# Kernel tuning notes

Measured on AMD Instinct MI355X. Metric: run time of the kernel, lower is better.

Reference implementation:

```python
import jax, jax.numpy as jnp
import numpy as np

B, S, D, H, DFF, NB = 32, 512, 256, 8, 1024, 2
L = NB + 2 * NB  # 2 blocks_1 + 4 blocks_2 = 6 layers, params stacked on axis 0
DK = D // H
NEG = jnp.float32(-1e32)


def _ln(x, s, b):
    mu = jnp.mean(x, -1, keepdims=True)
    var = jnp.mean((x - mu) ** 2, -1, keepdims=True)
    return (x - mu) * jax.lax.rsqrt(var + 1e-5) * s + b


def _attn(q, k, v, gamma, mask, zero_pad):
    # q,k,v: [B,H,S,DK]; mask: [1,1,S,S] bool; gamma: [H,1,1]
    scores = jnp.einsum('bhid,bhjd->bhij', q, k) / jnp.float32(np.sqrt(DK))
    # distance-decay effect (computed with no grad in the original)
    sc = jax.nn.softmax(jnp.where(mask, scores, NEG), axis=-1) * mask
    cum = jnp.cumsum(sc, axis=-1)
    tot = jnp.sum(sc, axis=-1, keepdims=True)
    idx = jnp.arange(S, dtype=jnp.float32)
    pos = jnp.abs(idx[None, :] - idx[:, None])[None, None]  # |i-j|
    dist = jax.lax.stop_gradient(jnp.sqrt(jnp.maximum((tot - cum) * pos, 0.0)))
    g = -jax.nn.softplus(gamma)[None]  # [1,H,1,1]
    eff = jnp.clip(jnp.exp(dist * g), 1e-5, 1e5)
    scores = jnp.where(mask, scores * eff, NEG)
    a = jax.nn.softmax(scores, axis=-1)
    if zero_pad:
        a = a.at[:, :, 0, :].set(0.0)
    return jnp.einsum('bhij,bhjd->bhid', a, v)


def _layer(i, mask_flag, q, k, v, apply_pos,
           Wk, bk, Wv, bv, Wo, bo, gammas, ln1_s, ln1_b, W1, b1, W2, b2, ln2_s, ln2_b):
    diag = 0 if mask_flag == 1 else -1  # mask=1: incl. diag; mask=0: strictly past
    mask = jnp.tril(jnp.ones((S, S), bool), diag)[None, None]
    to_h = lambda x, W, bb: (x @ W + bb).reshape(B, S, H, DK).transpose(0, 2, 1, 3)
    qh = to_h(q, Wk[i], bk[i])  # kq_same=True -> q uses k_linear
    kh = to_h(k, Wk[i], bk[i])
    vh = to_h(v, Wv[i], bv[i])
    o = _attn(qh, kh, vh, gammas[i], mask, zero_pad=(mask_flag == 0))
    o = o.transpose(0, 2, 1, 3).reshape(B, S, D) @ Wo[i] + bo[i]
    q = _ln(q + o, ln1_s[i], ln1_b[i])
    if apply_pos:
        f = jax.nn.relu(q @ W1[i] + b1[i]) @ W2[i] + b2[i]
        q = _ln(q + f, ln2_s[i], ln2_b[i])
    return q


def _forward(q_embed_data, qa_embed_data, *p):
    y, x = qa_embed_data, q_embed_data
    for i in range(NB):
        y = _layer(i, 1, y, y, y, True, *p)
    flag = True
    for j in range(2 * NB):
        i = NB + j
        if flag:
            x = _layer(i, 1, x, x, x, False, *p)
        else:
            x = _layer(i, 0, x, x, y, True, *p)
        flag = not flag
    return x


def setup_inputs() -> dict:
    key = jax.random.key(0)
    ks = jax.random.split(key, 9)
    sd = jnp.float32(1.0 / np.sqrt(D))
    sdf = jnp.float32(1.0 / np.sqrt(DFF))
    xb = float(np.sqrt(3.0))  # xavier bound for gammas (fan_in=fan_out=1)
    return {
        'q_embed_data': jax.random.normal(ks[0], (B, S, D), jnp.float32),
        'qa_embed_data': jax.random.normal(ks[1], (B, S, D), jnp.float32),
        'Wk': jax.random.normal(ks[2], (L, D, D), jnp.float32) * sd,
        'bk': jnp.zeros((L, D), jnp.float32),
        'Wv': jax.random.normal(ks[3], (L, D, D), jnp.float32) * sd,
        'bv': jnp.zeros((L, D), jnp.float32),
        'Wo': jax.random.normal(ks[4], (L, D, D), jnp.float32) * sd,
        'bo': jnp.zeros((L, D), jnp.float32),
        'gammas': jax.random.uniform(ks[5], (L, H, 1, 1), jnp.float32, -xb, xb),
        'ln1_s': jnp.ones((L, D), jnp.float32),
        'ln1_b': jnp.zeros((L, D), jnp.float32),
        'W1': jax.random.normal(ks[6], (L, D, DFF), jnp.float32) * sd,
        'b1': jnp.zeros((L, DFF), jnp.float32),
        'W2': jax.random.normal(ks[7], (L, DFF, D), jnp.float32) * sdf,
        'b2': jnp.zeros((L, D), jnp.float32),
        'ln2_s': jnp.ones((L, D), jnp.float32),
        'ln2_b': jnp.zeros((L, D), jnp.float32),
    }


def reference(q_embed_data, qa_embed_data, Wk, bk, Wv, bv, Wo, bo, gammas,
              ln1_s, ln1_b, W1, b1, W2, b2, ln2_s, ln2_b):
    return _forward(q_embed_data, qa_embed_data, Wk, bk, Wv, bv, Wo, bo, gammas,
                    ln1_s, ln1_b, W1, b1, W2, b2, ln2_s, ln2_b)
```

## Files before the change

### kernel.cpp

```cpp
#include <hip/hip_runtime.h>
#include <cstdint>
#include <cstddef>


#define AS1 __attribute__((address_space(1)))
#define AS3 __attribute__((address_space(3)))

typedef __bf16 bf16;
typedef __bf16 bf16x8 __attribute__((ext_vector_type(8)));
typedef __bf16 bf16x4 __attribute__((ext_vector_type(4)));
typedef __bf16 bf16x2 __attribute__((ext_vector_type(2)));
typedef float  f32x4  __attribute__((ext_vector_type(4)));
typedef float  f32x16 __attribute__((ext_vector_type(16)));
typedef unsigned int u32;

static constexpr int Mc = 32 * 512;

__global__ void cvt_copy2_kernel(const float* __restrict__ s0, float* __restrict__ da32,
                                 bf16* __restrict__ da16, const float* __restrict__ s1,
                                 float* __restrict__ db32, bf16* __restrict__ db16, int n4) {
  const float* s = blockIdx.y ? s1 : s0;
  float* d32 = blockIdx.y ? db32 : da32;
  bf16* d16 = blockIdx.y ? db16 : da16;
  int i = blockIdx.x * blockDim.x + threadIdx.x;
  if (i < n4) {
    float4 v = ((const float4*)s)[i];
    ((float4*)d32)[i] = v;
    bf16x4 hx = {(bf16)v.x, (bf16)v.y, (bf16)v.z, (bf16)v.w};
    ((bf16x4*)d16)[i] = hx;
  }
}

__global__ __launch_bounds__(256) void transpose_cvt_all(
    const float* __restrict__ Wk, const float* __restrict__ Wv, const float* __restrict__ Wo,
    const float* __restrict__ W1, const float* __restrict__ W2,
    bf16* __restrict__ Wkt, bf16* __restrict__ Wvt, bf16* __restrict__ Wot,
    bf16* __restrict__ W1t, bf16* __restrict__ W2t) {
  int z = blockIdx.z;
  int layer = z % 6, w = z / 6;
  const float* src; bf16* dst; int K, N;
  switch (w) {
    case 0: src = Wk; dst = Wkt; K = 256; N = 256; break;
    case 1: src = Wv; dst = Wvt; K = 256; N = 256; break;
    case 2: src = Wo; dst = Wot; K = 256; N = 256; break;
    case 3: src = W1; dst = W1t; K = 256; N = 1024; break;
    default: src = W2; dst = W2t; K = 1024; N = 256; break;
  }
  int k0 = blockIdx.x * 64, n0 = blockIdx.y * 64;
  if (k0 >= K || n0 >= N) return;
  src += (size_t)layer * K * N;
  dst += (size_t)layer * K * N;
  __shared__ bf16 t[64][68];
  int tid = threadIdx.x;
  int rr = tid >> 4;
  int c4 = (tid & 15) * 4;
#pragma unroll
  for (int p = 0; p < 4; ++p) {
    int k = rr + p * 16;
    float4 v = *(const float4*)(src + (size_t)(k0 + k) * N + n0 + c4);
    t[c4 + 0][k] = (bf16)v.x;
    t[c4 + 1][k] = (bf16)v.y;
    t[c4 + 2][k] = (bf16)v.z;
    t[c4 + 3][k] = (bf16)v.w;
  }
  __syncthreads();
#pragma unroll
  for (int p = 0; p < 4; ++p) {
    int nl = rr + p * 16;
    bf16x4 o4 = *(const bf16x4*)&t[nl][c4];
    *(bf16x4*)(dst + (size_t)(n0 + nl) * K + k0 + c4) = o4;
  }
}

template <int RELU, typename OUT_T>
__device__ __forceinline__ void gemm_body(
    const bf16* __restrict__ A, const bf16* __restrict__ Bt,
    const float* __restrict__ bias, OUT_T* __restrict__ C,
    int K, int N, int m0, int n0, bf16* As, bf16* Bs) {
  const int tid = threadIdx.x;
  const int lane = tid & 63;
  const int wid = tid >> 6;
  const int wm = (wid >> 1) * 64;
  const int wn = (wid & 1) * 64;
  f32x4 acc[4][4] = {};

  const int o1 = wid * 1024 + lane * 16;
  const int o2 = o1 + 4096;
  const int r1 = o1 >> 6, c1 = o1 & 63;
  const int r2 = o2 >> 6, c2 = o2 & 63;
  const char* Ab = (const char*)A;
  const char* Bb = (const char*)Bt;
  const size_t stride = (size_t)K * 2;

  auto stage_panel = [&](int panel, int kk) {
    const char* a1 = Ab + (size_t)(m0 + r1) * stride + (size_t)kk * 2 + c1;
    const char* a2 = Ab + (size_t)(m0 + r2) * stride + (size_t)kk * 2 + c2;
    const char* b1 = Bb + (size_t)(n0 + r1) * stride + (size_t)kk * 2 + c1;
    const char* b2 = Bb + (size_t)(n0 + r2) * stride + (size_t)kk * 2 + c2;
    char* ad = (char*)As + panel * 8192 + wid * 1024;
    char* bd = (char*)Bs + panel * 8192 + wid * 1024;
    __builtin_amdgcn_global_load_lds((const AS1 u32*)a1, (AS3 u32*)ad, 16, 0, 0);
    __builtin_amdgcn_global_load_lds((const AS1 u32*)a2, (AS3 u32*)(ad + 4096), 16, 0, 0);
    __builtin_amdgcn_global_load_lds((const AS1 u32*)b1, (AS3 u32*)bd, 16, 0, 0);
    __builtin_amdgcn_global_load_lds((const AS1 u32*)b2, (AS3 u32*)(bd + 4096), 16, 0, 0);
  };

  stage_panel(0, 0);
  stage_panel(1, 32);
  asm volatile("s_waitcnt vmcnt(0)" ::: "memory");
  __syncthreads();

  int cur = 0;
  for (int k0 = 0; k0 < K; k0 += 64) {
    if (k0 + 64 < K) {
      stage_panel((cur ^ 1) * 2, k0 + 64);
      stage_panel((cur ^ 1) * 2 + 1, k0 + 96);
    }
    const int rr = lane & 15;
    const int g8 = (lane >> 4) * 8;
#pragma unroll
    for (int s = 0; s < 2; ++s) {
      const int base = (cur * 2 + s) * 4096;
      bf16x8 af[4], bfr[4];
#pragma unroll
      for (int i = 0; i < 4; ++i) {
        af[i]  = *(const bf16x8*)&As[base + (wm + i * 16 + rr) * 32 + g8];
        bfr[i] = *(const bf16x8*)&Bs[base + (wn + i * 16 + rr) * 32 + g8];
      }
#pragma unroll
      for (int mi = 0; mi < 4; ++mi)
#pragma unroll
        for (int ni = 0; ni < 4; ++ni)
          acc[mi][ni] = __builtin_amdgcn_mfma_f32_16x16x32_bf16(af[mi], bfr[ni], acc[mi][ni], 0, 0, 0);
    }
    asm volatile("s_waitcnt vmcnt(0)" ::: "memory");
    __syncthreads();
    cur ^= 1;
  }

  const int rr = lane & 15;
  const int g4 = (lane >> 4) * 4;
  float bv[4];
#pragma unroll
  for (int ni = 0; ni < 4; ++ni) bv[ni] = bias[n0 + wn + ni * 16 + rr];
#pragma unroll
  for (int mi = 0; mi < 4; ++mi)
#pragma unroll
    for (int ni = 0; ni < 4; ++ni)
#pragma unroll
      for (int r = 0; r < 4; ++r) {
        float v = acc[mi][ni][r] + bv[ni];
        if (RELU) v = fmaxf(v, 0.f);
        int row = m0 + wm + mi * 16 + g4 + r;
        int col = n0 + wn + ni * 16 + rr;
        C[(size_t)row * N + col] = (OUT_T)v;
      }
}

__global__ __launch_bounds__(256) void gemm_kv_kernel(
    const bf16* __restrict__ A0, const bf16* __restrict__ Bt0,
    const float* __restrict__ b0, bf16* __restrict__ C0,
    const bf16* __restrict__ A1, const bf16* __restrict__ Bt1,
    const float* __restrict__ b1, bf16* __restrict__ C1, int K, int N) {
  __shared__ bf16 As[4 * 4096];
  __shared__ bf16 Bs[4 * 4096];
  int sel = blockIdx.y >> 1;
  gemm_body<0, bf16>(sel ? A1 : A0, sel ? Bt1 : Bt0, sel ? b1 : b0, sel ? C1 : C0,
                     K, N, blockIdx.x * 128, (blockIdx.y & 1) * 128, As, Bs);
}

template <int KSZ>
__global__ __launch_bounds__(512, 4) void gemm_ln_kernel(
    const bf16* __restrict__ A, const bf16* __restrict__ Bt,
    const float* __restrict__ bias, const float* __restrict__ resid,
    const float* __restrict__ lns, const float* __restrict__ lnb,
    float* __restrict__ out32, bf16* __restrict__ out16) {
  __shared__ bf16 As[2 * 32 * 32];
  __shared__ bf16 Bs[2 * 256 * 32];
  __shared__ float wsum[8][16][2];
  __shared__ float stats[32][2];
  const int tid = threadIdx.x, lane = tid & 63, wid = tid >> 6;
  const int m0 = blockIdx.x * 32;
  const int wr = wid >> 2, wc = wid & 3;
  f32x4 acc[4] = {};
  const char* Ab = (const char*)A;
  const char* Bb = (const char*)Bt;
  const size_t stride = (size_t)KSZ * 2;

  auto stage = [&](int buf, int kk) {
    if (wid < 2) {
      int off = wid * 1024 + lane * 16;
      const char* a1 = Ab + (size_t)(m0 + (off >> 6)) * stride + (size_t)kk * 2 + (off & 63);
      __builtin_amdgcn_global_load_lds((const AS1 u32*)a1,
                                       (AS3 u32*)((char*)As + buf * 2048 + wid * 1024), 16, 0, 0);
    }
    int off1 = wid * 2048 + lane * 16;
    int off2 = off1 + 1024;
    const char* b1 = Bb + (size_t)(off1 >> 6) * stride + (size_t)kk * 2 + (off1 & 63);
    const char* b2 = Bb + (size_t)(off2 >> 6) * stride + (size_t)kk * 2 + (off2 & 63);
    char* bd = (char*)Bs + buf * 16384 + wid * 2048;
    __builtin_amdgcn_global_load_lds((const AS1 u32*)b1, (AS3 u32*)bd, 16, 0, 0);
    __builtin_amdgcn_global_load_lds((const AS1 u32*)b2, (AS3 u32*)(bd + 1024), 16, 0, 0);
  };

  stage(0, 0);
  asm volatile("s_waitcnt vmcnt(0)" ::: "memory");
  __syncthreads();

  int cur = 0;
  for (int k0 = 0; k0 < KSZ; k0 += 32) {
    if (k0 + 32 < KSZ) stage(cur ^ 1, k0 + 32);
    const int rr = lane & 15, g8 = (lane >> 4) * 8;
    bf16x8 af = *(const bf16x8*)&As[cur * 1024 + (wr * 16 + rr) * 32 + g8];
    bf16x8 bfr[4];
#pragma unroll
    for (int ni = 0; ni < 4; ++ni)
      bfr[ni] = *(const bf16x8*)&Bs[cur * 8192 + (wc * 64 + ni * 16 + rr) * 32 + g8];
#pragma unroll
    for (int ni = 0; ni < 4; ++ni)
      acc[ni] = __builtin_amdgcn_mfma_f32_16x16x32_bf16(af, bfr[ni], acc[ni], 0, 0, 0);
    asm volatile("s_waitcnt vmcnt(0)" ::: "memory");
    __syncthreads();
    cur ^= 1;
  }

  const int rr = lane & 15, g4 = (lane >> 4) * 4;
  float bv[4], scv[4], biv[4];
  int col[4];
#pragma unroll
  for (int ni = 0; ni < 4; ++ni) {
    col[ni] = wc * 64 + ni * 16 + rr;
    bv[ni] = bias[col[ni]];
    scv[ni] = lns[col[ni]];
    biv[ni] = lnb[col[ni]];
  }
  float v[4][4];
#pragma unroll
  for (int r = 0; r < 4; ++r) {
    int grow = m0 + wr * 16 + g4 + r;
#pragma unroll
    for (int ni = 0; ni < 4; ++ni)
      v[ni][r] = acc[ni][r] + bv[ni] + resid[(size_t)grow * 256 + col[ni]];
  }
#pragma unroll
  for (int r = 0; r < 4; ++r) {
    float s1 = (v[0][r] + v[1][r]) + (v[2][r] + v[3][r]);
    float s2 = (v[0][r] * v[0][r] + v[1][r] * v[1][r]) + (v[2][r] * v[2][r] + v[3][r] * v[3][r]);
#pragma unroll
    for (int off = 8; off; off >>= 1) {
      s1 += __shfl_xor(s1, off);
      s2 += __shfl_xor(s2, off);
    }
    if (rr == 0) {
      int lrow = wr * 16 + g4 + r;
      wsum[wid][lrow & 15][0] = s1;
      wsum[wid][lrow & 15][1] = s2;
    }
  }
  __syncthreads();
  if (tid < 32) {
    int row = tid;
    int band = row >> 4;
    float s1 = 0.f, s2 = 0.f;
#pragma unroll
    for (int k = 0; k < 4; ++k) {
      s1 += wsum[band * 4 + k][row & 15][0];
      s2 += wsum[band * 4 + k][row & 15][1];
    }
    float mu = s1 * (1.f / 256.f);
    float var = s2 * (1.f / 256.f) - mu * mu;
    stats[row][0] = mu;
    stats[row][1] = rsqrtf(var + 1e-5f);
  }
  __syncthreads();
#pragma unroll
  for (int r = 0; r < 4; ++r) {
    int lrow = wr * 16 + g4 + r;
    int grow = m0 + lrow;
    float mu = stats[lrow][0], rs = stats[lrow][1];
#pragma unroll
    for (int ni = 0; ni < 4; ++ni) {
      float y = (v[ni][r] - mu) * rs * scv[ni] + biv[ni];
      out32[(size_t)grow * 256 + col[ni]] = y;
      out16[(size_t)grow * 256 + col[ni]] = (bf16)y;
    }
  }
}

__global__ __launch_bounds__(1024, 4) void gemm_ln_ffn_kernel(
    const bf16* __restrict__ A, const bf16* __restrict__ Bt,
    const float* __restrict__ bias, const float* __restrict__ resid,
    const float* __restrict__ lns, const float* __restrict__ lnb,
    const bf16* __restrict__ W1t, const float* __restrict__ b1,
    const bf16* __restrict__ W2t, const float* __restrict__ b2,
    const float* __restrict__ ln2s, const float* __restrict__ ln2b,
    float* __restrict__ out32, bf16* __restrict__ out16) {
  __shared__ bf16 As[2 * 4096];
  __shared__ bf16 Bs[2 * 16384];
  __shared__ bf16 vL[64 * 264];
  __shared__ bf16 hch[64 * 264];
  __shared__ float wsum[16][16][2];
  __shared__ float stats[64][2];
  const int tid = threadIdx.x, lane = tid & 63, wid = tid >> 6;
  const int m0 = blockIdx.x * 64;
  const int wr = wid >> 2, wc = wid & 3;
  const int rr = lane & 15, g4 = (lane >> 4) * 4, g8 = (lane >> 4) * 8;
  const int g = lane >> 4;
  const char* Ab = (const char*)A;
  const char* Bb = (const char*)Bt;
  const size_t strideA = 512;
  const size_t strideW1 = 512;
  const size_t strideW2 = 2048;

  int col[4];
#pragma unroll
  for (int ni = 0; ni < 4; ++ni) col[ni] = wc * 64 + ni * 16 + rr;

  auto stageA = [&](int kk, int buf) {
    if (wid < 8) {
      int cp = wid * 64 + lane;
      int cl = cp ^ ((cp >> 3) & 7);
      int row = cl >> 3, gq = cl & 7;
      const char* a1 = Ab + (size_t)(m0 + row) * strideA + (size_t)kk * 2 + gq * 16;
      __builtin_amdgcn_global_load_lds((const AS1 u32*)a1,
                                       (AS3 u32*)((char*)As + buf * 8192 + cp * 16), 16, 0, 0);
    }
  };
  auto stageB = [&](const char* Wb, size_t strideB, int rbase, int kk, int buf) {
#pragma unroll
    for (int j = 0; j < 2; ++j) {
      int cp = wid * 128 + j * 64 + lane;
      int cl = cp ^ ((cp >> 3) & 7);
      int row = cl >> 3, gq = cl & 7;
      const char* b1p = Wb + (size_t)(rbase + row) * strideB + (size_t)kk * 2 + gq * 16;
      __builtin_amdgcn_global_load_lds((const AS1 u32*)b1p,
                                       (AS3 u32*)((char*)Bs + buf * 32768 + cp * 16), 16, 0, 0);
    }
  };
  auto breadB = [&](int buf, int nrow, int s) -> bf16x8 {
    int cb = nrow * 8 + s * 4 + g;
    int cs = cb ^ (nrow & 7);
    return *(const bf16x8*)&Bs[buf * 16384 + cs * 8];
  };
  auto areadA = [&](int buf, int nrow, int s) -> bf16x8 {
    int cb = nrow * 8 + s * 4 + g;
    int cs = cb ^ (nrow & 7);
    return *(const bf16x8*)&As[buf * 4096 + cs * 8];
  };

  f32x4 acc[4] = {};
  stageA(0, 0);
  stageB(Bb, strideA, 0, 0, 0);
  {
    int cur = 0;
    for (int k0 = 0; k0 < 256; k0 += 64) {
      const bool pf = (k0 + 64 < 256);
      if (pf) {
        stageA(k0 + 64, cur ^ 1);
        stageB(Bb, strideA, 0, k0 + 64, cur ^ 1);
        if (wid < 8) asm volatile("s_waitcnt vmcnt(3)" ::: "memory");
        else         asm volatile("s_waitcnt vmcnt(2)" ::: "memory");
      } else {
        asm volatile("s_waitcnt vmcnt(0)" ::: "memory");
      }
      __builtin_amdgcn_s_barrier();
      __builtin_amdgcn_sched_barrier(0);
#pragma unroll
      for (int s = 0; s < 2; ++s) {
        bf16x8 af = areadA(cur, wr * 16 + rr, s);
        bf16x8 bfr[4];
#pragma unroll
        for (int ni = 0; ni < 4; ++ni)
          bfr[ni] = breadB(cur, wc * 64 + ni * 16 + rr, s);
#pragma unroll
        for (int ni = 0; ni < 4; ++ni)
          acc[ni] = __builtin_amdgcn_mfma_f32_16x16x32_bf16(af, bfr[ni], acc[ni], 0, 0, 0);
      }
      __builtin_amdgcn_sched_barrier(0);
      __builtin_amdgcn_s_barrier();
      cur ^= 1;
    }
  }

  float y[4][4];
  {
    float bv[4], scv[4], biv[4];
#pragma unroll
    for (int ni = 0; ni < 4; ++ni) {
      bv[ni] = bias[col[ni]];
      scv[ni] = lns[col[ni]];
      biv[ni] = lnb[col[ni]];
    }
    float v[4][4];
#pragma unroll
    for (int r = 0; r < 4; ++r) {
      int grow = m0 + wr * 16 + g4 + r;
#pragma unroll
      for (int ni = 0; ni < 4; ++ni)
        v[ni][r] = acc[ni][r] + bv[ni] + resid[(size_t)grow * 256 + col[ni]];
    }
#pragma unroll
    for (int r = 0; r < 4; ++r) {
      float s1 = (v[0][r] + v[1][r]) + (v[2][r] + v[3][r]);
      float s2 = (v[0][r] * v[0][r] + v[1][r] * v[1][r]) + (v[2][r] * v[2][r] + v[3][r] * v[3][r]);
#pragma unroll
      for (int off = 8; off; off >>= 1) {
        s1 += __shfl_xor(s1, off);
        s2 += __shfl_xor(s2, off);
      }
      if (rr == 0) {
        wsum[wid][g4 + r][0] = s1;
        wsum[wid][g4 + r][1] = s2;
      }
    }
    __syncthreads();
    if (tid < 64) {
      int row = tid;
      int band = row >> 4;
      float s1 = 0.f, s2 = 0.f;
#pragma unroll
      for (int k = 0; k < 4; ++k) {
        s1 += wsum[band * 4 + k][row & 15][0];
        s2 += wsum[band * 4 + k][row & 15][1];
      }
      float mu = s1 * (1.f / 256.f);
      float var = s2 * (1.f / 256.f) - mu * mu;
      stats[row][0] = mu;
      stats[row][1] = rsqrtf(var + 1e-5f);
    }
    __syncthreads();
#pragma unroll
    for (int r = 0; r < 4; ++r) {
      int lrow = wr * 16 + g4 + r;
      float mu = stats[lrow][0], rs = stats[lrow][1];
#pragma unroll
      for (int ni = 0; ni < 4; ++ni) {
        float yy = (v[ni][r] - mu) * rs * scv[ni] + biv[ni];
        y[ni][r] = yy;
        vL[lrow * 264 + col[ni]] = (bf16)yy;
      }
    }
  }
  __syncthreads();

  const char* W1b = (const char*)W1t;
  const char* W2b = (const char*)W2t;
  f32x4 acc2[4] = {};

  for (int nb = 0; nb < 4; ++nb) {
    f32x4 acc1[4] = {};
    stageB(W1b, strideW1, nb * 256, 0, 0);
    {
      int cur = 0;
      for (int k0 = 0; k0 < 256; k0 += 64) {
        const bool pf = (k0 + 64 < 256);
        if (pf) {
          stageB(W1b, strideW1, nb * 256, k0 + 64, cur ^ 1);
          asm volatile("s_waitcnt vmcnt(2)" ::: "memory");
        } else {
          asm volatile("s_waitcnt vmcnt(0)" ::: "memory");
        }
        __builtin_amdgcn_s_barrier();
        __builtin_amdgcn_sched_barrier(0);
#pragma unroll
        for (int s = 0; s < 2; ++s) {
          bf16x8 af = *(const bf16x8*)&vL[(wr * 16 + rr) * 264 + k0 + s * 32 + g8];
          bf16x8 bfr[4];
#pragma unroll
          for (int ni = 0; ni < 4; ++ni)
            bfr[ni] = breadB(cur, wc * 64 + ni * 16 + rr, s);
#pragma unroll
          for (int ni = 0; ni < 4; ++ni)
            acc1[ni] = __builtin_amdgcn_mfma_f32_16x16x32_bf16(af, bfr[ni], acc1[ni], 0, 0, 0);
        }
        __builtin_amdgcn_sched_barrier(0);
        __builtin_amdgcn_s_barrier();
        cur ^= 1;
      }
    }
#pragma unroll
    for (int ni = 0; ni < 4; ++ni) {
      float bb = b1[nb * 256 + col[ni]];
#pragma unroll
      for (int r = 0; r < 4; ++r) {
        int lrow = wr * 16 + g4 + r;
        hch[lrow * 264 + col[ni]] = (bf16)fmaxf(acc1[ni][r] + bb, 0.f);
      }
    }
    __syncthreads();

    stageB(W2b, strideW2, 0, nb * 256, 0);
    {
      int cur = 0;
      for (int k0 = 0; k0 < 256; k0 += 64) {
        const bool pf = (k0 + 64 < 256);
        if (pf) {
          stageB(W2b, strideW2, 0, nb * 256 + k0 + 64, cur ^ 1);
          asm volatile("s_waitcnt vmcnt(2)" ::: "memory");
        } else {
          asm volatile("s_waitcnt vmcnt(0)" ::: "memory");
        }
        __builtin_amdgcn_s_barrier();
        __builtin_amdgcn_sched_barrier(0);
#pragma unroll
        for (int s = 0; s < 2; ++s) {
          bf16x8 af = *(const bf16x8*)&hch[(wr * 16 + rr) * 264 + k0 + s * 32 + g8];
          bf16x8 bfr[4];
#pragma unroll
          for (int ni = 0; ni < 4; ++ni)
            bfr[ni] = breadB(cur, wc * 64 + ni * 16 + rr, s);
#pragma unroll
          for (int ni = 0; ni < 4; ++ni)
            acc2[ni] = __builtin_amdgcn_mfma_f32_16x16x32_bf16(af, bfr[ni], acc2[ni], 0, 0, 0);
        }
        __builtin_amdgcn_sched_barrier(0);
        __builtin_amdgcn_s_barrier();
        cur ^= 1;
      }
    }
    __syncthreads();
  }

  {
    float bv[4], scv[4], biv[4];
#pragma unroll
    for (int ni = 0; ni < 4; ++ni) {
      bv[ni] = b2[col[ni]];
      scv[ni] = ln2s[col[ni]];
      biv[ni] = ln2b[col[ni]];
    }
    float v[4][4];
#pragma unroll
    for (int r = 0; r < 4; ++r)
#pragma unroll
      for (int ni = 0; ni < 4; ++ni)
        v[ni][r] = y[ni][r] + acc2[ni][r] + bv[ni];
#pragma unroll
    for (int r = 0; r < 4; ++r) {
      float s1 = (v[0][r] + v[1][r]) + (v[2][r] + v[3][r]);
      float s2 = (v[0][r] * v[0][r] + v[1][r] * v[1][r]) + (v[2][r] * v[2][r] + v[3][r] * v[3][r]);
#pragma unroll
      for (int off = 8; off; off >>= 1) {
        s1 += __shfl_xor(s1, off);
        s2 += __shfl_xor(s2, off);
      }
      if (rr == 0) {
        wsum[wid][g4 + r][0] = s1;
        wsum[wid][g4 + r][1] = s2;
      }
    }
    __syncthreads();
    if (tid < 64) {
      int row = tid;
      int band = row >> 4;
      float s1 = 0.f, s2 = 0.f;
#pragma unroll
      for (int k = 0; k < 4; ++k) {
        s1 += wsum[band * 4 + k][row & 15][0];
        s2 += wsum[band * 4 + k][row & 15][1];
      }
      float mu = s1 * (1.f / 256.f);
      float var = s2 * (1.f / 256.f) - mu * mu;
      stats[row][0] = mu;
      stats[row][1] = rsqrtf(var + 1e-5f);
    }
    __syncthreads();
#pragma unroll
    for (int r = 0; r < 4; ++r) {
      int lrow = wr * 16 + g4 + r;
      int grow = m0 + lrow;
      float mu = stats[lrow][0], rs = stats[lrow][1];
#pragma unroll
      for (int ni = 0; ni < 4; ++ni) {
        float yy = (v[ni][r] - mu) * rs * scv[ni] + biv[ni];
        out32[(size_t)grow * 256 + col[ni]] = yy;
        out16[(size_t)grow * 256 + col[ni]] = (bf16)yy;
      }
    }
  }
}

static constexpr int LDK = 34;
static constexpr int LDV = 534;
static constexpr float LOG2E = 1.4426950408889634f;
static constexpr float KSC = 0.17677669529663687f * LOG2E;

__device__ __forceinline__ int jloc(int r, int hi) { return (r & 3) + 8 * (r >> 2) + 4 * hi; }

__device__ __forceinline__ u32 pkbf(float x, float y) {
  bf16x2 t = {(bf16)x, (bf16)y};
  return __builtin_bit_cast(u32, t);
}

__device__ __forceinline__ void plswap(u32& a, u32& b) {
  asm volatile("v_permlane32_swap_b32 %0, %1" : "+v"(a), "+v"(b));
}

__device__ __forceinline__ f32x16 qk_tile(const bf16* Klds, int jbase, int lq,
                                          const bf16x8& qf0, const bf16x8& qf1, int hi) {
  const bf16x8 ka0 = *(const bf16x8*)&Klds[(jbase + lq) * LDK + hi * 8];
  const bf16x8 ka1 = *(const bf16x8*)&Klds[(jbase + lq) * LDK + 16 + hi * 8];
  f32x16 c = {};
  c = __builtin_amdgcn_mfma_f32_32x32x16_bf16(ka0, qf0, c, 0, 0, 0);
  c = __builtin_amdgcn_mfma_f32_32x32x16_bf16(ka1, qf1, c, 0, 0, 0);
  return c;
}

template <bool MASKED>
__device__ __forceinline__ void tileA(const f32x16& c, int jbase, int hi, int qlim, float& tot) {
  float t[4] = {0.f, 0.f, 0.f, 0.f};
#pragma unroll
  for (int q2 = 0; q2 < 4; ++q2)
#pragma unroll
    for (int p = 0; p < 4; ++p) {
      const int r = q2 * 4 + p;
      float e = __builtin_amdgcn_exp2f(c[r] * KSC);
      if (MASKED) {
        int j = jbase + 8 * q2 + 4 * hi + p;
        if (j > qlim) e = 0.f;
      }
      t[q2] += e;
    }
  tot += (t[0] + t[1]) + (t[2] + t[3]);
}

template <bool MASKED>
__device__ __forceinline__ void tileB(const f32x16& c, int jbase, int lq, int hi,
                                      int qlim, float itot, float gneg2, float posf,
                                      const bf16* Vt, float& run, float& sum2, f32x16& pvacc) {
  float su2[16], lcs[16], G[4];
#pragma unroll
  for (int q2 = 0; q2 < 4; ++q2) {
    float a = 0.f;
#pragma unroll
    for (int p = 0; p < 4; ++p) {
      const int r = q2 * 4 + p;
      su2[r] = c[r] * KSC;
      float e = __builtin_amdgcn_exp2f(su2[r]);
      if (MASKED) {
        int j = jbase + 8 * q2 + 4 * hi + p;
        if (j > qlim) e = 0.f;
      }
      a += e;
      lcs[r] = a;
    }
    G[q2] = a;
  }
  float Po[4];
#pragma unroll
  for (int q2 = 0; q2 < 4; ++q2) Po[q2] = __shfl_xor(G[q2], 32);
  float base[4];
  {
    float pre = run;
#pragma unroll
    for (int q2 = 0; q2 < 4; ++q2) {
      base[q2] = pre + (hi ? Po[q2] : 0.f);
      pre += G[q2] + Po[q2];
    }
    run = pre;
  }
#pragma unroll
  for (int cc = 0; cc < 2; ++cc) {
    float pv[8];
#pragma unroll
    for (int q2s = 0; q2s < 2; ++q2s) {
      const int q2 = cc * 2 + q2s;
#pragma unroll
      for (int p = 0; p < 4; ++p) {
        const int r = q2 * 4 + p;
        float cum = base[q2] + lcs[r];
        float pos = posf - (float)(8 * q2 + p);
        float d2 = fmaxf(__builtin_fmaf(-cum, itot, 1.f) * pos, 0.f);
        float dist = __builtin_amdgcn_sqrtf(d2);
        float eff = fmaxf(__builtin_amdgcn_exp2f(dist * gneg2), 1e-5f);
        float t = __builtin_amdgcn_exp2f(su2[r] * eff);
        if (MASKED) {
          int j = jbase + 8 * q2 + 4 * hi + p;
          if (j > qlim) t = 0.f;
        }
        pv[q2s * 4 + p] = t;
      }
    }
    sum2 += ((pv[0] + pv[1]) + (pv[2] + pv[3])) + ((pv[4] + pv[5]) + (pv[6] + pv[7]));
    u32 a0 = pkbf(pv[0], pv[1]);
    u32 a1 = pkbf(pv[2], pv[3]);
    u32 b0 = pkbf(pv[4], pv[5]);
    u32 b1 = pkbf(pv[6], pv[7]);
    plswap(a0, b0);
    plswap(a1, b1);
    uint4 fq; fq.x = a0; fq.y = a1; fq.z = b0; fq.w = b1;
    bf16x8 pa = __builtin_bit_cast(bf16x8, fq);
    bf16x8 vb = *(const bf16x8*)&Vt[(size_t)lq * LDV + jbase + cc * 16 + hi * 8];
    pvacc = __builtin_amdgcn_mfma_f32_32x32x16_bf16(pa, vb, pvacc, 0, 0, 0);
  }
}

__global__ __launch_bounds__(1024, 4) void attn_kernel(
    const bf16* __restrict__ kh, const bf16* __restrict__ vh,
    const float* __restrict__ gam, bf16* __restrict__ o, int incl_diag) {
  __shared__ bf16 Klds[512 * LDK];
  __shared__ bf16 Vt[32 * LDV];
  __shared__ float exA[8][32];
  __shared__ float exB[8][32];
  __shared__ float s2A[8][32];
  __shared__ float pvp[8][32][32];

  const int tid = threadIdx.x;
  const int lane = tid & 63;
  const int wid = tid >> 6;
  const int bh = blockIdx.x;
  const int b = bh >> 3, h = bh & 7;
  const bf16* kbase = kh + ((size_t)b * 4096 + h) * 32;
  const bf16* vbase = vh + ((size_t)b * 4096 + h) * 32;
  bf16* obase = o + ((size_t)b * 4096 + h) * 32;

#pragma unroll
  for (int it = 0; it < 2; ++it) {
    int t = it * 1024 + tid;
    int j = t >> 2, cc = t & 3;
    bf16x8 kv8 = *(const bf16x8*)(kbase + (size_t)j * 256 + cc * 8);
    *(bf16x8*)&Klds[j * LDK + cc * 8] = kv8;
  }
  {
    int u = tid & 255;
    int cg = tid >> 8;
    const bf16* vb = vbase + (size_t)(2 * u) * 256 + cg * 8;
    bf16x8 r0 = *(const bf16x8*)(vb);
    bf16x8 r1 = *(const bf16x8*)(vb + 256);
#pragma unroll
    for (int e = 0; e < 8; ++e) {
      bf16x2 w2 = {r0[e], r1[e]};
      *(bf16x2*)&Vt[(size_t)(cg * 8 + e) * LDV + 2 * u] = w2;
    }
  }
  __syncthreads();

  float gm = gam[h];
  float gneg = -(fmaxf(gm, 0.f) + log1pf(__expf(-fabsf(gm))));
  const float gneg2 = gneg * LOG2E;
  const int lq = lane & 31;
  const int hi = lane >> 5;

  const int p = wid & 7;
  const bool front = wid < 8;
  const int f = 7 - p;
  const int qbHi = 15 - p;
  const int ntHi = 16 - p;
  const int q0Hi = qbHi * 32;
  const int qrHi = q0Hi + lq;
  const int qlimHi = incl_diag ? qrHi : qrHi - 1;
  const int q0Lo = p * 32;
  const int qrLo = q0Lo + lq;
  const int qlimLo = incl_diag ? qrLo : qrLo - 1;

  const bf16x8 qfH0 = *(const bf16x8*)&Klds[(q0Hi + lq) * LDK + hi * 8];
  const bf16x8 qfH1 = *(const bf16x8*)&Klds[(q0Hi + lq) * LDK + 16 + hi * 8];

  float totLo = 0.f, S = 0.f;
  if (front) {
    const bf16x8 qfL0 = *(const bf16x8*)&Klds[(q0Lo + lq) * LDK + hi * 8];
    const bf16x8 qfL1 = *(const bf16x8*)&Klds[(q0Lo + lq) * LDK + 16 + hi * 8];
    for (int jt = 0; jt < p; ++jt) {
      f32x16 c = qk_tile(Klds, jt * 32, lq, qfL0, qfL1, hi);
      tileA<false>(c, jt * 32, hi, qlimLo, totLo);
    }
    {
      f32x16 c = qk_tile(Klds, q0Lo, lq, qfL0, qfL1, hi);
      tileA<true>(c, q0Lo, hi, qlimLo, totLo);
    }
    totLo += __shfl_xor(totLo, 32);
    for (int jt = 0; jt < f; ++jt) {
      f32x16 c = qk_tile(Klds, jt * 32, lq, qfH0, qfH1, hi);
      tileA<false>(c, jt * 32, hi, qlimHi, S);
    }
    S += __shfl_xor(S, 32);
    if (lane < 32) exA[p][lq] = S;
  } else {
    for (int jt = f; jt < ntHi - 1; ++jt) {
      f32x16 c = qk_tile(Klds, jt * 32, lq, qfH0, qfH1, hi);
      tileA<false>(c, jt * 32, hi, qlimHi, S);
    }
    {
      f32x16 c = qk_tile(Klds, q0Hi, lq, qfH0, qfH1, hi);
      tileA<true>(c, q0Hi, hi, qlimHi, S);
    }
    S += __shfl_xor(S, 32);
    if (lane < 32) exB[p][lq] = S;
  }
  __syncthreads();
  const float SA = exA[p][lq];
  const float SB = exB[p][lq];
  const float totHi = SA + SB;
  const float itotHi = totHi > 0.f ? 1.f / totHi : 0.f;

  f32x16 pvHi = {};
  float sum2Hi = 0.f;
  if (front) {
    const bf16x8 qfL0 = *(const bf16x8*)&Klds[(q0Lo + lq) * LDK + hi * 8];
    const bf16x8 qfL1 = *(const bf16x8*)&Klds[(q0Lo + lq) * LDK + 16 + hi * 8];
    const float itotLo = totLo > 0.f ? 1.f / totLo : 0.f;
    f32x16 pvLo = {};
    float sum2Lo = 0.f, run = 0.f;
    float posf = (float)(qrLo - 4 * hi);
    for (int jt = 0; jt < p; ++jt) {
      f32x16 c = qk_tile(Klds, jt * 32, lq, qfL0, qfL1, hi);
      tileB<false>(c, jt * 32, lq, hi, qlimLo, itotLo, gneg2, posf, Vt, run, sum2Lo, pvLo);
      posf -= 32.f;
    }
    {
      f32x16 c = qk_tile(Klds, q0Lo, lq, qfL0, qfL1, hi);
      tileB<true>(c, q0Lo, lq, hi, qlimLo, itotLo, gneg2, posf, Vt, run, sum2Lo, pvLo);
    }
    sum2Lo += __shfl_xor(sum2Lo, 32);
    const float inv2Lo = sum2Lo > 0.f ? 1.f / sum2Lo : 0.f;
#pragma unroll
    for (int r = 0; r < 16; ++r) {
      int qv = jloc(r, hi);
      float iv = __shfl(inv2Lo, qv);
      obase[(size_t)(q0Lo + qv) * 256 + lq] = (bf16)(pvLo[r] * iv);
    }
    run = 0.f;
    posf = (float)(qrHi - 4 * hi);
    for (int jt = 0; jt < f; ++jt) {
      f32x16 c = qk_tile(Klds, jt * 32, lq, qfH0, qfH1, hi);
      tileB<false>(c, jt * 32, lq, hi, qlimHi, itotHi, gneg2, posf, Vt, run, sum2Hi, pvHi);
      posf -= 32.f;
    }
    sum2Hi += __shfl_xor(sum2Hi, 32);
    if (lane < 32) s2A[p][lq] = sum2Hi;
#pragma unroll
    for (int r = 0; r < 16; ++r) pvp[p][jloc(r, hi)][lq] = pvHi[r];
  } else {
    float run = SA;
    float posf = (float)(qrHi - 4 * hi - 32 * f);
    for (int jt = f; jt < ntHi - 1; ++jt) {
      f32x16 c = qk_tile(Klds, jt * 32, lq, qfH0, qfH1, hi);
      tileB<false>(c, jt * 32, lq, hi, qlimHi, itotHi, gneg2, posf, Vt, run, sum2Hi, pvHi);
      posf -= 32.f;
    }
    {
      f32x16 c = qk_tile(Klds, q0Hi, lq, qfH0, qfH1, hi);
      tileB<true>(c, q0Hi, lq, hi, qlimHi, itotHi, gneg2, posf, Vt, run, sum2Hi, pvHi);
    }
    sum2Hi += __shfl_xor(sum2Hi, 32);
  }
  __syncthreads();
  if (!front) {
    const float s2 = s2A[p][lq] + sum2Hi;
    const float inv2 = s2 > 0.f ? 1.f / s2 : 0.f;
#pragma unroll
    for (int r = 0; r < 16; ++r) {
      int qv = jloc(r, hi);
      float iv = __shfl(inv2, qv);
      float val = pvHi[r] + pvp[p][qv][lq];
      obase[(size_t)(q0Hi + qv) * 256 + lq] = (bf16)(val * iv);
    }
  }
}

extern "C" void kernel_launch(void* const* d_in, const int* in_sizes, int n_in,
                              void* d_out, int out_size, void* d_ws, size_t ws_size,
                              hipStream_t stream) {
  const float* q_embed  = (const float*)d_in[0];
  const float* qa_embed = (const float*)d_in[1];
  const float* Wk = (const float*)d_in[2];
  const float* bk = (const float*)d_in[3];
  const float* Wv = (const float*)d_in[4];
  const float* bv = (const float*)d_in[5];
  const float* Wo = (const float*)d_in[6];
  const float* bo = (const float*)d_in[7];
  const float* gammas = (const float*)d_in[8];
  const float* ln1_s = (const float*)d_in[9];
  const float* ln1_b = (const float*)d_in[10];
  const float* W1 = (const float*)d_in[11];
  const float* b1 = (const float*)d_in[12];
  const float* W2 = (const float*)d_in[13];
  const float* b2 = (const float*)d_in[14];
  const float* ln2_s = (const float*)d_in[15];
  const float* ln2_b = (const float*)d_in[16];
  float* out = (float*)d_out;

  char* ws = (char*)d_ws;
  float* y32 = (float*)(ws);
  float* x32 = (float*)(ws + ((size_t)16 << 20));
  bf16* y16  = (bf16*)(ws + ((size_t)32 << 20));
  bf16* x16  = (bf16*)(ws + ((size_t)40 << 20));
  bf16* khb  = (bf16*)(ws + ((size_t)48 << 20));
  bf16* vhb  = (bf16*)(ws + ((size_t)56 << 20));
  bf16* o16  = (bf16*)(ws + ((size_t)64 << 20));
  bf16* Wkt  = (bf16*)(ws + ((size_t)122 << 20));
  bf16* Wvt  = Wkt + 6 * 65536;
  bf16* Wot  = Wvt + 6 * 65536;
  bf16* W1t  = Wot + 6 * 65536;
  bf16* W2t  = W1t + 6 * 262144;

  transpose_cvt_all<<<dim3(16, 16, 30), 256, 0, stream>>>(Wk, Wv, Wo, W1, W2,
                                                          Wkt, Wvt, Wot, W1t, W2t);
  cvt_copy2_kernel<<<dim3(4096, 2), 256, 0, stream>>>(q_embed, x32, x16,
                                                      qa_embed, y32, y16, Mc * 256 / 4);

  for (int i = 0; i < 6; ++i) {
    const bool first = (i < 2);
    const bool strict = (i == 3 || i == 5);
    const bool pos = first || strict;
    bf16* in16 = first ? y16 : x16;
    bf16* v16  = (first || strict) ? y16 : x16;
    float* res32 = first ? y32 : x32;

    gemm_kv_kernel<<<dim3(128, 4), 256, 0, stream>>>(
        in16, Wkt + (size_t)i * 65536, bk + i * 256, khb,
        v16, Wvt + (size_t)i * 65536, bv + i * 256, vhb, 256, 256);
    attn_kernel<<<256, 1024, 0, stream>>>(khb, vhb, gammas + i * 8, o16, strict ? 0 : 1);
    if (pos) {
      float* fin = (i == 5) ? out : res32;
      gemm_ln_ffn_kernel<<<256, 1024, 0, stream>>>(
          o16, Wot + (size_t)i * 65536, bo + i * 256, res32,
          ln1_s + i * 256, ln1_b + i * 256,
          W1t + (size_t)i * 262144, b1 + i * 1024,
          W2t + (size_t)i * 262144, b2 + i * 256,
          ln2_s + i * 256, ln2_b + i * 256, fin, in16);
    } else {
      gemm_ln_kernel<256><<<512, 512, 0, stream>>>(
          o16, Wot + (size_t)i * 65536, bo + i * 256, res32,
          ln1_s + i * 256, ln1_b + i * 256, res32, in16);
    }
  }
}
```

Before: 523.7 us.

## Split attention across two blocks per head and read K from global memory

Each (batch, head) attention block of 1024 threads becomes two 512-thread blocks. Each block takes an interleaved half of the query tiles (pi + 2p), giving a 2x larger grid with smaller blocks. The K tile is no longer staged in LDS; QK fragments are read straight from global memory, relying on cache hits. This removes the K staging pass and its LDS footprint, which can raise occupancy, at the cost of repeated global/L2 loads for K. The pack-and-permlane helper code is also inlined, with no change in behaviour.

```diff
diff --git a/kernel.cpp b/kernel.cpp
--- a/kernel.cpp
+++ b/kernel.cpp
@@ -580,26 +580,17 @@
   }
 }
 
-static constexpr int LDK = 34;
 static constexpr int LDV = 534;
 static constexpr float LOG2E = 1.4426950408889634f;
 static constexpr float KSC = 0.17677669529663687f * LOG2E;
 
 __device__ __forceinline__ int jloc(int r, int hi) { return (r & 3) + 8 * (r >> 2) + 4 * hi; }
 
-__device__ __forceinline__ u32 pkbf(float x, float y) {
-  bf16x2 t = {(bf16)x, (bf16)y};
-  return __builtin_bit_cast(u32, t);
-}
-
-__device__ __forceinline__ void plswap(u32& a, u32& b) {
-  asm volatile("v_permlane32_swap_b32 %0, %1" : "+v"(a), "+v"(b));
-}
-
-__device__ __forceinline__ f32x16 qk_tile(const bf16* Klds, int jbase, int lq,
-                                          const bf16x8& qf0, const bf16x8& qf1, int hi) {
-  const bf16x8 ka0 = *(const bf16x8*)&Klds[(jbase + lq) * LDK + hi * 8];
-  const bf16x8 ka1 = *(const bf16x8*)&Klds[(jbase + lq) * LDK + 16 + hi * 8];
+__device__ __forceinline__ f32x16 qk_tile_g(const bf16* __restrict__ kbase, int jbase, int lq,
+                                            const bf16x8& qf0, const bf16x8& qf1, int hi) {
+  const bf16* kr = kbase + (size_t)(jbase + lq) * 256 + hi * 8;
+  bf16x8 ka0 = *(const bf16x8*)(kr);
+  bf16x8 ka1 = *(const bf16x8*)(kr + 16);
   f32x16 c = {};
   c = __builtin_amdgcn_mfma_f32_32x32x16_bf16(ka0, qf0, c, 0, 0, 0);
   c = __builtin_amdgcn_mfma_f32_32x32x16_bf16(ka1, qf1, c, 0, 0, 0);
@@ -682,12 +673,19 @@
       }
     }
     sum2 += ((pv[0] + pv[1]) + (pv[2] + pv[3])) + ((pv[4] + pv[5]) + (pv[6] + pv[7]));
-    u32 a0 = pkbf(pv[0], pv[1]);
-    u32 a1 = pkbf(pv[2], pv[3]);
-    u32 b0 = pkbf(pv[4], pv[5]);
-    u32 b1 = pkbf(pv[6], pv[7]);
-    plswap(a0, b0);
-    plswap(a1, b1);
+    u32 a0, a1, b0, b1;
+    {
+      bf16x2 t0 = {(bf16)pv[0], (bf16)pv[1]};
+      bf16x2 t1 = {(bf16)pv[2], (bf16)pv[3]};
+      bf16x2 t2 = {(bf16)pv[4], (bf16)pv[5]};
+      bf16x2 t3 = {(bf16)pv[6], (bf16)pv[7]};
+      a0 = __builtin_bit_cast(u32, t0);
+      a1 = __builtin_bit_cast(u32, t1);
+      b0 = __builtin_bit_cast(u32, t2);
+      b1 = __builtin_bit_cast(u32, t3);
+    }
+    asm volatile("v_permlane32_swap_b32 %0, %1" : "+v"(a0), "+v"(b0));
+    asm volatile("v_permlane32_swap_b32 %0, %1" : "+v"(a1), "+v"(b1));
     uint4 fq; fq.x = a0; fq.y = a1; fq.z = b0; fq.w = b1;
     bf16x8 pa = __builtin_bit_cast(bf16x8, fq);
     bf16x8 vb = *(const bf16x8*)&Vt[(size_t)lq * LDV + jbase + cc * 16 + hi * 8];
@@ -695,42 +693,38 @@
   }
 }
 
-__global__ __launch_bounds__(1024, 4) void attn_kernel(
+__global__ __launch_bounds__(512, 4) void attn_kernel(
     const bf16* __restrict__ kh, const bf16* __restrict__ vh,
     const float* __restrict__ gam, bf16* __restrict__ o, int incl_diag) {
-  __shared__ bf16 Klds[512 * LDK];
   __shared__ bf16 Vt[32 * LDV];
-  __shared__ float exA[8][32];
-  __shared__ float exB[8][32];
-  __shared__ float s2A[8][32];
-  __shared__ float pvp[8][32][32];
+  __shared__ float exA[4][32];
+  __shared__ float exB[4][32];
+  __shared__ float s2A[4][32];
+  __shared__ float pvp[4][32][32];
 
   const int tid = threadIdx.x;
   const int lane = tid & 63;
   const int wid = tid >> 6;
   const int bh = blockIdx.x;
+  const int pi = blockIdx.y;
   const int b = bh >> 3, h = bh & 7;
   const bf16* kbase = kh + ((size_t)b * 4096 + h) * 32;
   const bf16* vbase = vh + ((size_t)b * 4096 + h) * 32;
   bf16* obase = o + ((size_t)b * 4096 + h) * 32;
 
-#pragma unroll
-  for (int it = 0; it < 2; ++it) {
-    int t = it * 1024 + tid;
-    int j = t >> 2, cc = t & 3;
-    bf16x8 kv8 = *(const bf16x8*)(kbase + (size_t)j * 256 + cc * 8);
-    *(bf16x8*)&Klds[j * LDK + cc * 8] = kv8;
-  }
   {
     int u = tid & 255;
-    int cg = tid >> 8;
-    const bf16* vb = vbase + (size_t)(2 * u) * 256 + cg * 8;
-    bf16x8 r0 = *(const bf16x8*)(vb);
-    bf16x8 r1 = *(const bf16x8*)(vb + 256);
-#pragma unroll
-    for (int e = 0; e < 8; ++e) {
-      bf16x2 w2 = {r0[e], r1[e]};
-      *(bf16x2*)&Vt[(size_t)(cg * 8 + e) * LDV + 2 * u] = w2;
+#pragma unroll
+    for (int cgi = 0; cgi < 2; ++cgi) {
+      int cg = (tid >> 8) * 2 + cgi;
+      const bf16* vb = vbase + (size_t)(2 * u) * 256 + cg * 8;
+      bf16x8 r0 = *(const bf16x8*)(vb);
+      bf16x8 r1 = *(const bf16x8*)(vb + 256);
+#pragma unroll
+      for (int e = 0; e < 8; ++e) {
+        bf16x2 w2 = {r0[e], r1[e]};
+        *(bf16x2*)&Vt[(size_t)(cg * 8 + e) * LDV + 2 * u] = w2;
+      }
     }
   }
   __syncthreads();
@@ -741,47 +735,50 @@
   const int lq = lane & 31;
   const int hi = lane >> 5;
 
-  const int p = wid & 7;
-  const bool front = wid < 8;
-  const int f = 7 - p;
-  const int qbHi = 15 - p;
-  const int ntHi = 16 - p;
+  const int p = wid & 3;
+  const bool front = wid < 4;
+  const int f = 7 - 2 * p;
+  const int qbLo = pi + 2 * p;
+  const int qbHi = pi + 14 - 2 * p;
+  const int ntHi = qbHi + 1;
   const int q0Hi = qbHi * 32;
   const int qrHi = q0Hi + lq;
   const int qlimHi = incl_diag ? qrHi : qrHi - 1;
-  const int q0Lo = p * 32;
+  const int q0Lo = qbLo * 32;
   const int qrLo = q0Lo + lq;
   const int qlimLo = incl_diag ? qrLo : qrLo - 1;
 
-  const bf16x8 qfH0 = *(const bf16x8*)&Klds[(q0Hi + lq) * LDK + hi * 8];
-  const bf16x8 qfH1 = *(const bf16x8*)&Klds[(q0Hi + lq) * LDK + 16 + hi * 8];
+  const bf16* qrowH = kbase + (size_t)(q0Hi + lq) * 256 + hi * 8;
+  const bf16x8 qfH0 = *(const bf16x8*)(qrowH);
+  const bf16x8 qfH1 = *(const bf16x8*)(qrowH + 16);
 
   float totLo = 0.f, S = 0.f;
   if (front) {
-    const bf16x8 qfL0 = *(const bf16x8*)&Klds[(q0Lo + lq) * LDK + hi * 8];
-    const bf16x8 qfL1 = *(const bf16x8*)&Klds[(q0Lo + lq) * LDK + 16 + hi * 8];
-    for (int jt = 0; jt < p; ++jt) {
-      f32x16 c = qk_tile(Klds, jt * 32, lq, qfL0, qfL1, hi);
+    const bf16* qrowL = kbase + (size_t)(q0Lo + lq) * 256 + hi * 8;
+    const bf16x8 qfL0 = *(const bf16x8*)(qrowL);
+    const bf16x8 qfL1 = *(const bf16x8*)(qrowL + 16);
+    for (int jt = 0; jt < qbLo; ++jt) {
+      f32x16 c = qk_tile_g(kbase, jt * 32, lq, qfL0, qfL1, hi);
       tileA<false>(c, jt * 32, hi, qlimLo, totLo);
     }
     {
-      f32x16 c = qk_tile(Klds, q0Lo, lq, qfL0, qfL1, hi);
+      f32x16 c = qk_tile_g(kbase, q0Lo, lq, qfL0, qfL1, hi);
       tileA<true>(c, q0Lo, hi, qlimLo, totLo);
     }
     totLo += __shfl_xor(totLo, 32);
     for (int jt = 0; jt < f; ++jt) {
-      f32x16 c = qk_tile(Klds, jt * 32, lq, qfH0, qfH1, hi);
+      f32x16 c = qk_tile_g(kbase, jt * 32, lq, qfH0, qfH1, hi);
       tileA<false>(c, jt * 32, hi, qlimHi, S);
     }
     S += __shfl_xor(S, 32);
     if (lane < 32) exA[p][lq] = S;
   } else {
     for (int jt = f; jt < ntHi - 1; ++jt) {
-      f32x16 c = qk_tile(Klds, jt * 32, lq, qfH0, qfH1, hi);
+      f32x16 c = qk_tile_g(kbase, jt * 32, lq, qfH0, qfH1, hi);
       tileA<false>(c, jt * 32, hi, qlimHi, S);
     }
     {
-      f32x16 c = qk_tile(Klds, q0Hi, lq, qfH0, qfH1, hi);
+      f32x16 c = qk_tile_g(kbase, q0Hi, lq, qfH0, qfH1, hi);
       tileA<true>(c, q0Hi, hi, qlimHi, S);
     }
     S += __shfl_xor(S, 32);
@@ -796,19 +793,20 @@
   f32x16 pvHi = {};
   float sum2Hi = 0.f;
   if (front) {
-    const bf16x8 qfL0 = *(const bf16x8*)&Klds[(q0Lo + lq) * LDK + hi * 8];
-    const bf16x8 qfL1 = *(const bf16x8*)&Klds[(q0Lo + lq) * LDK + 16 + hi * 8];
+    const bf16* qrowL = kbase + (size_t)(q0Lo + lq) * 256 + hi * 8;
+    const bf16x8 qfL0 = *(const bf16x8*)(qrowL);
+    const bf16x8 qfL1 = *(const bf16x8*)(qrowL + 16);
     const float itotLo = totLo > 0.f ? 1.f / totLo : 0.f;
     f32x16 pvLo = {};
     float sum2Lo = 0.f, run = 0.f;
     float posf = (float)(qrLo - 4 * hi);
-    for (int jt = 0; jt < p; ++jt) {
-      f32x16 c = qk_tile(Klds, jt * 32, lq, qfL0, qfL1, hi);
+    for (int jt = 0; jt < qbLo; ++jt) {
+      f32x16 c = qk_tile_g(kbase, jt * 32, lq, qfL0, qfL1, hi);
       tileB<false>(c, jt * 32, lq, hi, qlimLo, itotLo, gneg2, posf, Vt, run, sum2Lo, pvLo);
       posf -= 32.f;
     }
     {
-      f32x16 c = qk_tile(Klds, q0Lo, lq, qfL0, qfL1, hi);
+      f32x16 c = qk_tile_g(kbase, q0Lo, lq, qfL0, qfL1, hi);
       tileB<true>(c, q0Lo, lq, hi, qlimLo, itotLo, gneg2, posf, Vt, run, sum2Lo, pvLo);
     }
     sum2Lo += __shfl_xor(sum2Lo, 32);
@@ -822,7 +820,7 @@
     run = 0.f;
     posf = (float)(qrHi - 4 * hi);
     for (int jt = 0; jt < f; ++jt) {
-      f32x16 c = qk_tile(Klds, jt * 32, lq, qfH0, qfH1, hi);
+      f32x16 c = qk_tile_g(kbase, jt * 32, lq, qfH0, qfH1, hi);
       tileB<false>(c, jt * 32, lq, hi, qlimHi, itotHi, gneg2, posf, Vt, run, sum2Hi, pvHi);
       posf -= 32.f;
     }
@@ -834,12 +832,12 @@
     float run = SA;
     float posf = (float)(qrHi - 4 * hi - 32 * f);
     for (int jt = f; jt < ntHi - 1; ++jt) {
-      f32x16 c = qk_tile(Klds, jt * 32, lq, qfH0, qfH1, hi);
+      f32x16 c = qk_tile_g(kbase, jt * 32, lq, qfH0, qfH1, hi);
       tileB<false>(c, jt * 32, lq, hi, qlimHi, itotHi, gneg2, posf, Vt, run, sum2Hi, pvHi);
       posf -= 32.f;
     }
     {
-      f32x16 c = qk_tile(Klds, q0Hi, lq, qfH0, qfH1, hi);
+      f32x16 c = qk_tile_g(kbase, q0Hi, lq, qfH0, qfH1, hi);
       tileB<true>(c, q0Hi, lq, hi, qlimHi, itotHi, gneg2, posf, Vt, run, sum2Hi, pvHi);
     }
     sum2Hi += __shfl_xor(sum2Hi, 32);
@@ -910,7 +908,7 @@
     gemm_kv_kernel<<<dim3(128, 4), 256, 0, stream>>>(
         in16, Wkt + (size_t)i * 65536, bk + i * 256, khb,
         v16, Wvt + (size_t)i * 65536, bv + i * 256, vhb, 256, 256);
-    attn_kernel<<<256, 1024, 0, stream>>>(khb, vhb, gammas + i * 8, o16, strict ? 0 : 1);
+    attn_kernel<<<dim3(256, 2), 512, 0, stream>>>(khb, vhb, gammas + i * 8, o16, strict ? 0 : 1);
     if (pos) {
       float* fin = (i == 5) ? out : res32;
       gemm_ln_ffn_kernel<<<256, 1024, 0, stream>>>(
```

After: 518.9 us (median of 2 runs). Within noise of the previous version (-0.9%).
